# Kernel tuning notes

Hardware: AMD Instinct MI355X
Metric: run time of the kernel (lower is better)

The kernel has to match this reference:

```python
import jax, jax.numpy as jnp
import numpy as np

ALPHA = 0.2  # LeakyReLU negative slope

B, K, F = 64, 100, 128   # batch, window_size (=num_nodes), n_features
E = 2 * K                 # embed_dim*2 = 200 (embed_dim defaults to window_size)


def setup_inputs() -> dict:
    key = jax.random.key(0)
    k1, k2, k3, k4, k5 = jax.random.split(key, 5)
    x = jax.random.normal(k1, (B, K, F), dtype=jnp.float32)
    # lin: Linear(2F -> E); store weight as (2F, E) so projection is x @ W
    W = jax.random.normal(k2, (2 * F, E), dtype=jnp.float32) * (1.0 / np.sqrt(2 * F))
    b = jax.random.normal(k3, (E,), dtype=jnp.float32) * 0.01
    # attention vector a: (E, 1) in torch; use (E,)
    a = jax.random.normal(k4, (E,), dtype=jnp.float32) * (1.414 / np.sqrt(E))
    bias = jax.random.normal(k5, (K, K), dtype=jnp.float32) * 0.01
    return {"x": x, "W": W, "b": b, "a": a, "bias": bias}


def reference(x, W, b, a, bias):
    F_ = x.shape[-1]
    # lin(concat(left, right)) == left @ W[:F] + right @ W[F:] + b;
    # compute the two projections once each instead of materializing the
    # (B, K, K, 2F) pairwise concat tensor.
    left_p = jnp.einsum('bkf,fe->bke', x, W[:F_])    # (B, K, E)
    right_p = jnp.einsum('bkf,fe->bke', x, W[F_:])   # (B, K, E)
    pre = left_p[:, :, None, :] + right_p[:, None, :, :] + b  # (B, K, K, E)
    act = jnp.where(pre > 0, pre, ALPHA * pre)                # LeakyReLU
    e = jnp.einsum('bije,e->bij', act, a) + bias              # (B, K, K)
    attention = jax.nn.softmax(e, axis=2)
    h = jax.nn.sigmoid(jnp.einsum('bij,bjf->bif', attention, x))  # (B, K, F)
    return h
```

## Files before the change

kernel.cpp:

```cpp
#include <hip/hip_runtime.h>

typedef _Float16 half_t;
typedef _Float16 h2 __attribute__((ext_vector_type(2)));
typedef unsigned int uint32;

#define K_ 100
#define F_ 128
#define E_ 200

#if defined(__has_builtin)
#if __has_builtin(__builtin_amdgcn_fdot2)
#define FDOT2(a,b,c) __builtin_amdgcn_fdot2((a),(b),(c),false)
#endif
#endif
#ifndef FDOT2
#define FDOT2(a,b,c) fmaf((float)(a).y,(float)(b).y, fmaf((float)(a).x,(float)(b).x,(c)))
#endif

__device__ __forceinline__ h2 bch2(uint32 u){ return __builtin_bit_cast(h2,u); }
__device__ __forceinline__ uint32 pkh2(float a, float b){
  h2 p; p.x=(half_t)a; p.y=(half_t)b; return __builtin_bit_cast(uint32,p);
}

#define LH_OFF 0
#define RH_OFF 640000
#define AH_OFF 1280000
#define WT_OFF 1280128

__global__ __launch_bounds__(256) void k_wt(
    const float* __restrict__ W, const float* __restrict__ avec,
    uint32* __restrict__ ws)
{
  const int t  = threadIdx.x;
  const int e0 = (int)blockIdx.x * 8;
  __shared__ float wtf[256 * 9];

  for (int u = t; u < 2048; u += 256) {
    int f = u >> 3, ec = u & 7;
    wtf[f * 9 + ec] = W[(size_t)f * E_ + e0 + ec];
  }
  if (blockIdx.x == 0 && t < 100)
    ws[AH_OFF + t] = pkh2(avec[2*t], avec[2*t+1]);
  __syncthreads();

  for (int u = t; u < 1024; u += 256) {
    int col16 = u >> 6, f2 = u & 63;
    int side = col16 >> 3, el = col16 & 7;
    int cu = side * 200 + e0 + el;
    int fbase = side * 128;
    ws[WT_OFF + (size_t)cu * 64 + f2] =
        pkh2(wtf[(fbase + 2*f2) * 9 + el], wtf[(fbase + 2*f2 + 1) * 9 + el]);
  }
}

__global__ __launch_bounds__(256) void k_proj(
    const float* __restrict__ x, const float* __restrict__ bvec,
    uint32* __restrict__ ws)
{
  const int t  = threadIdx.x;
  const int r0 = (int)blockIdx.x * 10;

  __shared__ __align__(16) uint32 xsh[10 * 64];

  for (int u = t; u < 640; u += 256) {
    int row = u >> 6, f2 = u & 63;
    const float* xp = x + (size_t)(r0 + row) * F_ + 2 * f2;
    xsh[row * 64 + f2] = pkh2(xp[0], xp[1]);
  }
  __syncthreads();

  if (t < 200) {
    const uint32* wt0 = ws + WT_OFF + (size_t)(2 * t) * 64;
    const uint32* wt1 = wt0 + 64;
    float acc0[10], acc1[10];
    #pragma unroll
    for (int r = 0; r < 10; ++r) { acc0[r] = 0.f; acc1[r] = 0.f; }
    #pragma unroll
    for (int q = 0; q < 16; ++q) {
      uint4 w0 = *(const uint4*)(wt0 + 4 * q);
      uint4 w1 = *(const uint4*)(wt1 + 4 * q);
      #pragma unroll
      for (int r = 0; r < 10; ++r) {
        uint4 xq = *(const uint4*)(xsh + r * 64 + 4 * q);
        acc0[r] = FDOT2(bch2(xq.x), bch2(w0.x), acc0[r]);
        acc0[r] = FDOT2(bch2(xq.y), bch2(w0.y), acc0[r]);
        acc0[r] = FDOT2(bch2(xq.z), bch2(w0.z), acc0[r]);
        acc0[r] = FDOT2(bch2(xq.w), bch2(w0.w), acc0[r]);
        acc1[r] = FDOT2(bch2(xq.x), bch2(w1.x), acc1[r]);
        acc1[r] = FDOT2(bch2(xq.y), bch2(w1.y), acc1[r]);
        acc1[r] = FDOT2(bch2(xq.z), bch2(w1.z), acc1[r]);
        acc1[r] = FDOT2(bch2(xq.w), bch2(w1.w), acc1[r]);
      }
    }
    const bool isR = (t >= 100);
    const int e2 = isR ? (t - 100) : t;
    if (isR) {
      float b0 = bvec[2 * e2], b1 = bvec[2 * e2 + 1];
      #pragma unroll
      for (int r = 0; r < 10; ++r) { acc0[r] += b0; acc1[r] += b1; }
    }
    uint32* dst = ws + (isR ? RH_OFF : LH_OFF);
    #pragma unroll
    for (int r = 0; r < 10; ++r)
      dst[(size_t)(r0 + r) * 100 + e2] = pkh2(acc0[r], acc1[r]);
  }
}

#define STEP(lu, au, r0u, r1u, r2u, r3u)                                   \
  do {                                                                     \
    h2 a2 = bch2(au); h2 l2 = bch2(lu); h2 rr, mm;                         \
    al = FDOT2(a2, l2, al);                                                \
    rr = bch2(r0u); ar[0] = FDOT2(a2, rr, ar[0]);                          \
    mm = __builtin_elementwise_min(l2 + rr, z2); acc[0] = FDOT2(a2, mm, acc[0]); \
    rr = bch2(r1u); ar[1] = FDOT2(a2, rr, ar[1]);                          \
    mm = __builtin_elementwise_min(l2 + rr, z2); acc[1] = FDOT2(a2, mm, acc[1]); \
    rr = bch2(r2u); ar[2] = FDOT2(a2, rr, ar[2]);                          \
    mm = __builtin_elementwise_min(l2 + rr, z2); acc[2] = FDOT2(a2, mm, acc[2]); \
    rr = bch2(r3u); ar[3] = FDOT2(a2, rr, ar[3]);                          \
    mm = __builtin_elementwise_min(l2 + rr, z2); acc[3] = FDOT2(a2, mm, acc[3]); \
  } while (0)

__global__ __launch_bounds__(640) void k_main(
    const float* __restrict__ x, const float* __restrict__ bias,
    const uint32* __restrict__ ws, float* __restrict__ out)
{
  const int t  = threadIdx.x;
  const int i0 = (int)blockIdx.x * 25;
  const int b  = (int)blockIdx.y;

  __shared__ float  att[2500];
  __shared__ uint32 att2[1250];
  __shared__ float  scratch[640];
  __shared__ float  rowmax[25], rowinv[25];

  const bool act = (t < 625);
  const int ti = act ? (t % 25) : 0;
  const int tj = act ? (t / 25) : 0;

  const uint32* Lrow = ws + LH_OFF + (size_t)(b*K_ + i0 + ti) * 100;
  const uint32* R0   = ws + RH_OFF + (size_t)(b*K_ + tj) * 100;
  const uint32* Ap   = ws + AH_OFF;

  float acc[4] = {0.f,0.f,0.f,0.f};
  float ar[4]  = {0.f,0.f,0.f,0.f};
  float al = 0.f;
  h2 z2; z2.x = (half_t)0; z2.y = (half_t)0;

  #pragma unroll
  for (int g = 0; g < 12; ++g) {
    const int ba = 8*g;
    uint4 La = *(const uint4*)(Lrow + ba),      Lb = *(const uint4*)(Lrow + ba + 4);
    uint4 Aa = *(const uint4*)(Ap + ba),        Ab = *(const uint4*)(Ap + ba + 4);
    uint4 R0a = *(const uint4*)(R0 + ba),       R0b = *(const uint4*)(R0 + ba + 4);
    uint4 R1a = *(const uint4*)(R0 + 2500+ba),  R1b = *(const uint4*)(R0 + 2500+ba+4);
    uint4 R2a = *(const uint4*)(R0 + 5000+ba),  R2b = *(const uint4*)(R0 + 5000+ba+4);
    uint4 R3a = *(const uint4*)(R0 + 7500+ba),  R3b = *(const uint4*)(R0 + 7500+ba+4);
    STEP(La.x, Aa.x, R0a.x, R1a.x, R2a.x, R3a.x);
    STEP(La.y, Aa.y, R0a.y, R1a.y, R2a.y, R3a.y);
    STEP(La.z, Aa.z, R0a.z, R1a.z, R2a.z, R3a.z);
    STEP(La.w, Aa.w, R0a.w, R1a.w, R2a.w, R3a.w);
    STEP(Lb.x, Ab.x, R0b.x, R1b.x, R2b.x, R3b.x);
    STEP(Lb.y, Ab.y, R0b.y, R1b.y, R2b.y, R3b.y);
    STEP(Lb.z, Ab.z, R0b.z, R1b.z, R2b.z, R3b.z);
    STEP(Lb.w, Ab.w, R0b.w, R1b.w, R2b.w, R3b.w);
  }
  {
    uint4 La = *(const uint4*)(Lrow + 96);
    uint4 Aa = *(const uint4*)(Ap + 96);
    uint4 R0a = *(const uint4*)(R0 + 96);
    uint4 R1a = *(const uint4*)(R0 + 2596);
    uint4 R2a = *(const uint4*)(R0 + 5096);
    uint4 R3a = *(const uint4*)(R0 + 7596);
    STEP(La.x, Aa.x, R0a.x, R1a.x, R2a.x, R3a.x);
    STEP(La.y, Aa.y, R0a.y, R1a.y, R2a.y, R3a.y);
    STEP(La.z, Aa.z, R0a.z, R1a.z, R2a.z, R3a.z);
    STEP(La.w, Aa.w, R0a.w, R1a.w, R2a.w, R3a.w);
  }

  float v[4];
  if (act) {
    #pragma unroll
    for (int s = 0; s < 4; ++s) {
      int j = tj + 25*s;
      float lv = al + ar[s] + bias[(i0 + ti)*K_ + j] - 0.8f*acc[s];
      v[s] = fminf(fmaxf(lv, -30000.f), 30000.f);
    }
  }

  {
    float m = -3.0e38f;
    if (act) {
      #pragma unroll
      for (int s = 0; s < 4; ++s) m = fmaxf(m, v[s]);
    }
    scratch[t] = m;
    __syncthreads();
    if (t < 25) {
      float mm = scratch[t];
      for (int k = 1; k < 25; ++k) mm = fmaxf(mm, scratch[t + 25*k]);
      rowmax[t] = mm;
    }
    __syncthreads();
    float ssum = 0.f;
    if (act) {
      float m2 = rowmax[ti];
      #pragma unroll
      for (int s = 0; s < 4; ++s) ssum += __expf(v[s] - m2);
    }
    scratch[t] = ssum;
    __syncthreads();
    if (t < 25) {
      float s2 = 0.f;
      for (int k = 0; k < 25; ++k) s2 += scratch[t + 25*k];
      rowinv[t] = 1.f / s2;
    }
    __syncthreads();
  }
  if (act) {
    float m = rowmax[ti], inv = rowinv[ti];
    #pragma unroll
    for (int s = 0; s < 4; ++s)
      att[ti*K_ + tj + 25*s] = __expf(v[s] - m) * inv;
  }
  __syncthreads();
  for (int u = t; u < 1250; u += 640) {
    int i = u / 50, jp = u - i*50;
    att2[i*50 + jp] = pkh2(att[i*K_ + 2*jp], att[i*K_ + 2*jp + 1]);
  }
  __syncthreads();

  {
    const int f = t & 127, ig = t >> 7;
    float z[5];
    #pragma unroll
    for (int m = 0; m < 5; ++m) z[m] = 0.f;
    const float* xb = x + (size_t)b*K_*F_ + f;
    for (int jp = 0; jp < 50; ++jp) {
      float x0 = xb[(size_t)(2*jp)*F_];
      float x1 = xb[(size_t)(2*jp+1)*F_];
      h2 xv = bch2(pkh2(x0, x1));
      #pragma unroll
      for (int m = 0; m < 5; ++m) {
        h2 av = bch2(att2[(ig + 5*m)*50 + jp]);
        z[m] = FDOT2(av, xv, z[m]);
      }
    }
    #pragma unroll
    for (int m = 0; m < 5; ++m) {
      int i = ig + 5*m;
      out[(size_t)(b*K_ + i0 + i)*F_ + f] = 1.f / (1.f + __expf(-z[m]));
    }
  }
}

extern "C" void kernel_launch(void* const* d_in, const int* in_sizes, int n_in,
                              void* d_out, int out_size, void* d_ws, size_t ws_size,
                              hipStream_t stream)
{
  const float* x    = (const float*)d_in[0];
  const float* W    = (const float*)d_in[1];
  const float* bvec = (const float*)d_in[2];
  const float* avec = (const float*)d_in[3];
  const float* bias = (const float*)d_in[4];
  float* out  = (float*)d_out;
  uint32* ws  = (uint32*)d_ws;

  k_wt  <<<dim3(25),    dim3(256), 0, stream>>>(W, avec, ws);
  k_proj<<<dim3(640),   dim3(256), 0, stream>>>(x, bvec, ws);
  k_main<<<dim3(4, 64), dim3(640), 0, stream>>>(x, bias, ws, out);
}
```

Before: 102.7 us.

## Precompute a·L and a·R dot terms in projection, shrink main blocks, pre-pack x pairs

Moves the per-row a·left and a·right dot products out of the pairwise inner loop into the projection kernel, where they are computed once per row and stored in workspace. This cuts two FDOT2s per step from the O(K²E) loop. The main kernel now uses 256-thread blocks covering 10 rows each, so the grid grows from 256 to 640 blocks for better occupancy. The projection kernel also writes x as half pairs interleaved along j, so the attention·x stage reads one packed word instead of two floats. Each block does a serial 100-element reduction by 20 threads, and the extra workspace writes add some traffic.

```diff
diff --git a/kernel.cpp b/kernel.cpp
--- a/kernel.cpp
+++ b/kernel.cpp
@@ -26,6 +26,9 @@
 #define RH_OFF 640000
 #define AH_OFF 1280000
 #define WT_OFF 1280128
+#define AL_OFF 1305728
+#define AR_OFF 1312128
+#define XJ_OFF 1318528
 
 __global__ __launch_bounds__(256) void k_wt(
     const float* __restrict__ W, const float* __restrict__ avec,
@@ -61,6 +64,7 @@
   const int r0 = (int)blockIdx.x * 10;
 
   __shared__ __align__(16) uint32 xsh[10 * 64];
+  __shared__ float red[20][100];
 
   for (int u = t; u < 640; u += 256) {
     int row = u >> 6, f2 = u & 63;
@@ -68,6 +72,16 @@
     xsh[row * 64 + f2] = pkh2(xp[0], xp[1]);
   }
   __syncthreads();
+
+  for (int u = t; u < 640; u += 256) {
+    int f = u & 127, lp = u >> 7;
+    uint32 u0 = xsh[(2*lp)     * 64 + (f >> 1)];
+    uint32 u1 = xsh[(2*lp + 1) * 64 + (f >> 1)];
+    int sh = (f & 1) * 16;
+    uint32 h0 = (u0 >> sh) & 0xffffu;
+    uint32 h1 = (u1 >> sh) & 0xffffu;
+    ws[XJ_OFF + (size_t)(r0/2 + lp) * 128 + f] = h0 | (h1 << 16);
+  }
 
   if (t < 200) {
     const uint32* wt0 = ws + WT_OFF + (size_t)(2 * t) * 64;
@@ -99,51 +113,57 @@
       #pragma unroll
       for (int r = 0; r < 10; ++r) { acc0[r] += b0; acc1[r] += b1; }
     }
+    h2 a2 = bch2(ws[AH_OFF + e2]);
     uint32* dst = ws + (isR ? RH_OFF : LH_OFF);
     #pragma unroll
-    for (int r = 0; r < 10; ++r)
-      dst[(size_t)(r0 + r) * 100 + e2] = pkh2(acc0[r], acc1[r]);
+    for (int r = 0; r < 10; ++r) {
+      uint32 pr = pkh2(acc0[r], acc1[r]);
+      dst[(size_t)(r0 + r) * 100 + e2] = pr;
+      red[(isR ? 10 : 0) + r][e2] = FDOT2(a2, bch2(pr), 0.f);
+    }
+  }
+  __syncthreads();
+
+  if (t < 20) {
+    float s = 0.f;
+    const float* rp = red[t];
+    for (int k = 0; k < 100; ++k) s += rp[k];
+    float* dstf = (float*)(ws + (t >= 10 ? AR_OFF : AL_OFF));
+    dstf[r0 + (t % 10)] = s;
   }
 }
 
 #define STEP(lu, au, r0u, r1u, r2u, r3u)                                   \
   do {                                                                     \
-    h2 a2 = bch2(au); h2 l2 = bch2(lu); h2 rr, mm;                         \
-    al = FDOT2(a2, l2, al);                                                \
-    rr = bch2(r0u); ar[0] = FDOT2(a2, rr, ar[0]);                          \
-    mm = __builtin_elementwise_min(l2 + rr, z2); acc[0] = FDOT2(a2, mm, acc[0]); \
-    rr = bch2(r1u); ar[1] = FDOT2(a2, rr, ar[1]);                          \
-    mm = __builtin_elementwise_min(l2 + rr, z2); acc[1] = FDOT2(a2, mm, acc[1]); \
-    rr = bch2(r2u); ar[2] = FDOT2(a2, rr, ar[2]);                          \
-    mm = __builtin_elementwise_min(l2 + rr, z2); acc[2] = FDOT2(a2, mm, acc[2]); \
-    rr = bch2(r3u); ar[3] = FDOT2(a2, rr, ar[3]);                          \
-    mm = __builtin_elementwise_min(l2 + rr, z2); acc[3] = FDOT2(a2, mm, acc[3]); \
+    h2 a2 = bch2(au); h2 l2 = bch2(lu); h2 mm;                             \
+    mm = __builtin_elementwise_min(l2 + bch2(r0u), z2); acc[0] = FDOT2(a2, mm, acc[0]); \
+    mm = __builtin_elementwise_min(l2 + bch2(r1u), z2); acc[1] = FDOT2(a2, mm, acc[1]); \
+    mm = __builtin_elementwise_min(l2 + bch2(r2u), z2); acc[2] = FDOT2(a2, mm, acc[2]); \
+    mm = __builtin_elementwise_min(l2 + bch2(r3u), z2); acc[3] = FDOT2(a2, mm, acc[3]); \
   } while (0)
 
-__global__ __launch_bounds__(640) void k_main(
+__global__ __launch_bounds__(256) void k_main(
     const float* __restrict__ x, const float* __restrict__ bias,
     const uint32* __restrict__ ws, float* __restrict__ out)
 {
   const int t  = threadIdx.x;
-  const int i0 = (int)blockIdx.x * 25;
+  const int i0 = (int)blockIdx.x * 10;
   const int b  = (int)blockIdx.y;
 
-  __shared__ float  att[2500];
-  __shared__ uint32 att2[1250];
-  __shared__ float  scratch[640];
-  __shared__ float  rowmax[25], rowinv[25];
-
-  const bool act = (t < 625);
-  const int ti = act ? (t % 25) : 0;
-  const int tj = act ? (t / 25) : 0;
+  __shared__ float  att[10 * 100];
+  __shared__ uint32 att2[10 * 50];
+  __shared__ float  scratch[256];
+  __shared__ float  rowmax[10], rowinv[10];
+
+  const bool act = (t < 250);
+  const int ti = act ? (t % 10) : 0;
+  const int tj = act ? (t / 10) : 0;
 
   const uint32* Lrow = ws + LH_OFF + (size_t)(b*K_ + i0 + ti) * 100;
   const uint32* R0   = ws + RH_OFF + (size_t)(b*K_ + tj) * 100;
   const uint32* Ap   = ws + AH_OFF;
 
   float acc[4] = {0.f,0.f,0.f,0.f};
-  float ar[4]  = {0.f,0.f,0.f,0.f};
-  float al = 0.f;
   h2 z2; z2.x = (half_t)0; z2.y = (half_t)0;
 
   #pragma unroll
@@ -179,10 +199,13 @@
 
   float v[4];
   if (act) {
+    const float* ALf = (const float*)(ws + AL_OFF);
+    const float* ARf = (const float*)(ws + AR_OFF);
+    float al = ALf[b*K_ + i0 + ti];
     #pragma unroll
     for (int s = 0; s < 4; ++s) {
       int j = tj + 25*s;
-      float lv = al + ar[s] + bias[(i0 + ti)*K_ + j] - 0.8f*acc[s];
+      float lv = al + ARf[b*K_ + j] + bias[(i0 + ti)*K_ + j] - 0.8f*acc[s];
       v[s] = fminf(fmaxf(lv, -30000.f), 30000.f);
     }
   }
@@ -195,9 +218,9 @@
     }
     scratch[t] = m;
     __syncthreads();
-    if (t < 25) {
+    if (t < 10) {
       float mm = scratch[t];
-      for (int k = 1; k < 25; ++k) mm = fmaxf(mm, scratch[t + 25*k]);
+      for (int k = 1; k < 25; ++k) mm = fmaxf(mm, scratch[t + 10*k]);
       rowmax[t] = mm;
     }
     __syncthreads();
@@ -209,9 +232,9 @@
     }
     scratch[t] = ssum;
     __syncthreads();
-    if (t < 25) {
+    if (t < 10) {
       float s2 = 0.f;
-      for (int k = 0; k < 25; ++k) s2 += scratch[t + 25*k];
+      for (int k = 0; k < 25; ++k) s2 += scratch[t + 10*k];
       rowinv[t] = 1.f / s2;
     }
     __syncthreads();
@@ -223,7 +246,7 @@
       att[ti*K_ + tj + 25*s] = __expf(v[s] - m) * inv;
   }
   __syncthreads();
-  for (int u = t; u < 1250; u += 640) {
+  for (int u = t; u < 500; u += 256) {
     int i = u / 50, jp = u - i*50;
     att2[i*50 + jp] = pkh2(att[i*K_ + 2*jp], att[i*K_ + 2*jp + 1]);
   }
@@ -231,23 +254,21 @@
 
   {
     const int f = t & 127, ig = t >> 7;
+    const uint32* XJ = ws + XJ_OFF + (size_t)(b*50) * 128;
     float z[5];
     #pragma unroll
     for (int m = 0; m < 5; ++m) z[m] = 0.f;
-    const float* xb = x + (size_t)b*K_*F_ + f;
     for (int jp = 0; jp < 50; ++jp) {
-      float x0 = xb[(size_t)(2*jp)*F_];
-      float x1 = xb[(size_t)(2*jp+1)*F_];
-      h2 xv = bch2(pkh2(x0, x1));
+      h2 xv = bch2(XJ[jp*128 + f]);
       #pragma unroll
       for (int m = 0; m < 5; ++m) {
-        h2 av = bch2(att2[(ig + 5*m)*50 + jp]);
+        h2 av = bch2(att2[(ig*5 + m)*50 + jp]);
         z[m] = FDOT2(av, xv, z[m]);
       }
     }
     #pragma unroll
     for (int m = 0; m < 5; ++m) {
-      int i = ig + 5*m;
+      int i = ig*5 + m;
       out[(size_t)(b*K_ + i0 + i)*F_ + f] = 1.f / (1.f + __expf(-z[m]));
     }
   }
@@ -265,7 +286,7 @@
   float* out  = (float*)d_out;
   uint32* ws  = (uint32*)d_ws;
 
-  k_wt  <<<dim3(25),    dim3(256), 0, stream>>>(W, avec, ws);
-  k_proj<<<dim3(640),   dim3(256), 0, stream>>>(x, bvec, ws);
-  k_main<<<dim3(4, 64), dim3(640), 0, stream>>>(x, bias, ws, out);
-}
+  k_wt  <<<dim3(25),     dim3(256), 0, stream>>>(W, avec, ws);
+  k_proj<<<dim3(640),    dim3(256), 0, stream>>>(x, bvec, ws);
+  k_main<<<dim3(10, 64), dim3(256), 0, stream>>>(x, bias, ws, out);
+}
```

Measured after the change: 106.0 us. +3.3%, slower.
